# Kernel optimization log

Measured on AMD Instinct MI355X. Metric: run time of the kernel, lower is better.

## Reference

```python
import jax, jax.numpy as jnp
import numpy as np

LAMBDA = 0.9
T = 8192


def setup_inputs() -> dict:
    key = jax.random.key(0)
    k1, k2, k3, k4 = jax.random.split(key, 4)
    return {
        "log_pfs": jax.random.normal(k1, (T,), dtype=jnp.float32),
        "log_pbs": jax.random.normal(k2, (T,), dtype=jnp.float32),
        "log_flows": jax.random.normal(k3, (T + 1,), dtype=jnp.float32),
        "log_reward": jax.random.normal(k4, (), dtype=jnp.float32),
    }


def reference(log_pfs, log_pbs, log_flows, log_reward):
    t = log_pfs.shape[0]
    # terminal flow is replaced by the log reward (log_flows has T+1 entries)
    lfr = log_flows.at[t].set(log_reward)
    zero = jnp.zeros((1,), dtype=log_pfs.dtype)
    cpf = jnp.concatenate([zero, jnp.cumsum(log_pfs)])  # [T+1], cpf[j]-cpf[i] = sum log_pfs[i:j]
    cpb = jnp.concatenate([zero, jnp.cumsum(log_pbs)])
    # balance(i,j) = lfr[i] + (cpf[j]-cpf[i]) - lfr[j] - (cpb[j]-cpb[i]) = D[i] - D[j]
    d = lfr - cpf + cpb  # [T+1]; then balance = d[i]-d[j]+ (cpf[j]-cpf[i]) ... simplify directly:
    d = lfr + (cpb - cpf)  # balance(i,j) = d[i] - d[j]
    idx = jnp.arange(t + 1)
    length = idx[None, :] - idx[:, None]  # j - i
    mask = length > 0
    w = jnp.where(mask, jnp.asarray(LAMBDA, log_pfs.dtype) ** length.astype(log_pfs.dtype), 0.0)
    bal = d[:, None] - d[None, :]
    total = jnp.sum(w * bal * bal)
    wsum = jnp.sum(w)
    return jnp.where(wsum > 0, total / wsum, total)
```

## Files before the change

### kernel.cpp

```cpp
#include <hip/hip_runtime.h>


#define TT 8192
#define NTH 1024
#define LAM 0.9
#define LOG2LAM_F (-0.15200309344504995f)

constexpr double dpow(double b, long e) {
  double r = 1.0;
  for (long i = 0; i < e; ++i) r *= b;
  return r;
}

constexpr float M8F[7] = {
    (float)dpow(LAM, 8),   (float)dpow(LAM, 16),  (float)dpow(LAM, 32),
    (float)dpow(LAM, 64),  (float)dpow(LAM, 128), (float)dpow(LAM, 256),
    (float)dpow(LAM, 512)};

__global__ __launch_bounds__(NTH) void subtb_fused_kernel(
    const float* __restrict__ log_pfs,
    const float* __restrict__ log_pbs,
    const float* __restrict__ log_flows,
    const float* __restrict__ log_reward,
    float* __restrict__ out, double wsum) {
  const int tid  = threadIdx.x;
  const int lane = tid & 63;
  const int wid  = tid >> 6;
  const int base = tid * 8;

  __shared__ double wtot1[16];
  __shared__ float  wtot2[16];
  __shared__ float  rt1[16], rt2[16];

  const float4* pf4 = (const float4*)(log_pfs + base);
  const float4* pb4 = (const float4*)(log_pbs + base);
  const float4* fl4 = (const float4*)(log_flows + base);
  float4 a0 = pf4[0], a1 = pf4[1];
  float4 b0 = pb4[0], b1 = pb4[1];
  float4 f0 = fl4[0], f1 = fl4[1];
  float fa[8] = {a0.x, a0.y, a0.z, a0.w, a1.x, a1.y, a1.z, a1.w};
  float fb[8] = {b0.x, b0.y, b0.z, b0.w, b1.x, b1.y, b1.z, b1.w};
  float ff[8] = {f0.x, f0.y, f0.z, f0.w, f1.x, f1.y, f1.z, f1.w};

  double lexcl[8];
  double run = 0.0;
#pragma unroll
  for (int r = 0; r < 8; ++r) {
    lexcl[r] = run;
    run += (double)fb[r] - (double)fa[r];
  }
  double x = run;
#pragma unroll
  for (int off = 1; off < 64; off <<= 1) {
    double u = __shfl_up(x, off, 64);
    if (lane >= off) x += u;
  }
  if (lane == 63) wtot1[wid] = x;
  __syncthreads();
  double wexcl = 0.0;
  for (int w = 0; w < wid; ++w) wexcl += wtot1[w];
  const double texcl = wexcl + (x - run);

  float dvf[8];
#pragma unroll
  for (int r = 0; r < 8; ++r) dvf[r] = (float)((double)ff[r] + texcl + lexcl[r]);

  float bl = 0.0f;
#pragma unroll
  for (int r = 0; r < 8; ++r) bl = 0.9f * (bl + dvf[r]);

  float xw = __shfl_up(bl, 1, 64);
  if (lane < 1) xw = 0.0f;
#pragma unroll
  for (int b = 0; b < 6; ++b) {
    const int off = 1 << b;
    float u = __shfl_up(xw, off, 64);
    if (lane >= off) xw += M8F[b] * u;
  }
  if (lane == 63) wtot2[wid] = bl + M8F[0] * xw;
  __syncthreads();
  float Cw = 0.0f;
  for (int w = 0; w < wid; ++w) Cw = M8F[6] * Cw + wtot2[w];
  float c = __builtin_amdgcn_exp2f(8.0f * LOG2LAM_F * (float)lane) * Cw + xw;

  float t1 = 0.0f, t2 = 0.0f;
  float pj = __builtin_amdgcn_exp2f(LOG2LAM_F * (float)base);
  float qj = __builtin_amdgcn_exp2f(LOG2LAM_F * (float)(TT - base));
  const float invl = 1.0f / 0.9f;
#pragma unroll
  for (int r = 0; r < 8; ++r) {
    const float dr = dvf[r];
    t1 += dr * dr * (2.0f - qj - pj);
    t2 += dr * c;
    c = 0.9f * (c + dr);
    pj *= 0.9f;
    qj *= invl;
  }
  if (tid == NTH - 1) {
    const double dT = (double)log_reward[0] + (wexcl + x);
    t1 += (float)(dT * dT);
    t2 += (float)dT * c;
  }

#pragma unroll
  for (int off = 32; off > 0; off >>= 1) {
    t1 += __shfl_down(t1, off, 64);
    t2 += __shfl_down(t2, off, 64);
  }
  if (lane == 0) { rt1[wid] = t1; rt2[wid] = t2; }
  __syncthreads();
  if (tid == 0) {
    double s1 = 0.0, s2 = 0.0;
    for (int w = 0; w < 16; ++w) { s1 += (double)rt1[w]; s2 += (double)rt2[w]; }
    const double total = (LAM / (1.0 - LAM)) * s1 - 2.0 * s2;
    out[0] = (float)(total / wsum);
  }
}

extern "C" void kernel_launch(void* const* d_in, const int* in_sizes, int n_in,
                              void* d_out, int out_size, void* d_ws, size_t ws_size,
                              hipStream_t stream) {
  const float* log_pfs    = (const float*)d_in[0];
  const float* log_pbs    = (const float*)d_in[1];
  const float* log_flows  = (const float*)d_in[2];
  const float* log_reward = (const float*)d_in[3];
  float* out = (float*)d_out;

  double wsum = 0.0, lp = 1.0;
  for (int k = 1; k <= TT; ++k) {
    lp *= LAM;
    wsum += (double)(TT + 1 - k) * lp;
  }

  subtb_fused_kernel<<<1, NTH, 0, stream>>>(log_pfs, log_pbs, log_flows, log_reward, out, wsum);
}
```

Before: 9.949 us.

## Merge the two block scans into one fp32 triple scan

Replaces the double-precision prefix scan followed by a second decayed scan with a single pass. Three quantities (plain prefix sum S and decayed sums U of the differences and V of the flows) are scanned together in fp32, and the carry c is rebuilt algebraically as V + 9S − 10U. This removes one __syncthreads phase, the serial dependency between the scans, and the slow FP64 shuffles and adds. In exchange there are three times the fp32 shuffles, and accumulating the prefix in fp32 with the c recombination may lose accuracy through cancellation.

```diff
diff --git a/kernel.cpp b/kernel.cpp
--- a/kernel.cpp
+++ b/kernel.cpp
@@ -3,7 +3,10 @@
 
 #define TT 8192
 #define NTH 1024
-#define LAM 0.9
+#define LAMF 0.9f
+#define INVLF (1.0f / 0.9f)
+#define C1F 9.0f
+#define C2F 10.0f
 #define LOG2LAM_F (-0.15200309344504995f)
 
 constexpr double dpow(double b, long e) {
@@ -13,9 +16,9 @@
 }
 
 constexpr float M8F[7] = {
-    (float)dpow(LAM, 8),   (float)dpow(LAM, 16),  (float)dpow(LAM, 32),
-    (float)dpow(LAM, 64),  (float)dpow(LAM, 128), (float)dpow(LAM, 256),
-    (float)dpow(LAM, 512)};
+    (float)dpow(0.9, 8),   (float)dpow(0.9, 16),  (float)dpow(0.9, 32),
+    (float)dpow(0.9, 64),  (float)dpow(0.9, 128), (float)dpow(0.9, 256),
+    (float)dpow(0.9, 512)};
 
 __global__ __launch_bounds__(NTH) void subtb_fused_kernel(
     const float* __restrict__ log_pfs,
@@ -28,9 +31,8 @@
   const int wid  = tid >> 6;
   const int base = tid * 8;
 
-  __shared__ double wtot1[16];
-  __shared__ float  wtot2[16];
-  __shared__ float  rt1[16], rt2[16];
+  __shared__ float wS[16], wU[16], wV[16];
+  __shared__ float rt1[16], rt2[16];
 
   const float4* pf4 = (const float4*)(log_pfs + base);
   const float4* pb4 = (const float4*)(log_pbs + base);
@@ -38,68 +40,73 @@
   float4 a0 = pf4[0], a1 = pf4[1];
   float4 b0 = pb4[0], b1 = pb4[1];
   float4 f0 = fl4[0], f1 = fl4[1];
-  float fa[8] = {a0.x, a0.y, a0.z, a0.w, a1.x, a1.y, a1.z, a1.w};
-  float fb[8] = {b0.x, b0.y, b0.z, b0.w, b1.x, b1.y, b1.z, b1.w};
+  float fe[8] = {b0.x - a0.x, b0.y - a0.y, b0.z - a0.z, b0.w - a0.w,
+                 b1.x - a1.x, b1.y - a1.y, b1.z - a1.z, b1.w - a1.w};
   float ff[8] = {f0.x, f0.y, f0.z, f0.w, f1.x, f1.y, f1.z, f1.w};
 
-  double lexcl[8];
-  double run = 0.0;
+  float lexcl[8];
+  float runS = 0.0f;
+#pragma unroll
+  for (int r = 0; r < 8; ++r) { lexcl[r] = runS; runS += fe[r]; }
+  float blU = 0.0f;
+  float blV = 0.0f;
 #pragma unroll
   for (int r = 0; r < 8; ++r) {
-    lexcl[r] = run;
-    run += (double)fb[r] - (double)fa[r];
+    blU = LAMF * (blU + fe[r]);
+    blV = LAMF * (blV + ff[r]);
   }
-  double x = run;
-#pragma unroll
-  for (int off = 1; off < 64; off <<= 1) {
-    double u = __shfl_up(x, off, 64);
-    if (lane >= off) x += u;
-  }
-  if (lane == 63) wtot1[wid] = x;
-  __syncthreads();
-  double wexcl = 0.0;
-  for (int w = 0; w < wid; ++w) wexcl += wtot1[w];
-  const double texcl = wexcl + (x - run);
 
-  float dvf[8];
-#pragma unroll
-  for (int r = 0; r < 8; ++r) dvf[r] = (float)((double)ff[r] + texcl + lexcl[r]);
-
-  float bl = 0.0f;
-#pragma unroll
-  for (int r = 0; r < 8; ++r) bl = 0.9f * (bl + dvf[r]);
-
-  float xw = __shfl_up(bl, 1, 64);
-  if (lane < 1) xw = 0.0f;
+  float xS = runS;
+  float xU = __shfl_up(blU, 1, 64);
+  float xV = __shfl_up(blV, 1, 64);
+  if (lane == 0) { xU = 0.0f; xV = 0.0f; }
 #pragma unroll
   for (int b = 0; b < 6; ++b) {
     const int off = 1 << b;
-    float u = __shfl_up(xw, off, 64);
-    if (lane >= off) xw += M8F[b] * u;
+    float uS = __shfl_up(xS, off, 64);
+    float uU = __shfl_up(xU, off, 64);
+    float uV = __shfl_up(xV, off, 64);
+    if (lane >= off) {
+      xS += uS;
+      xU += M8F[b] * uU;
+      xV += M8F[b] * uV;
+    }
   }
-  if (lane == 63) wtot2[wid] = bl + M8F[0] * xw;
+  if (lane == 63) {
+    wS[wid] = xS;
+    wU[wid] = blU + M8F[0] * xU;
+    wV[wid] = blV + M8F[0] * xV;
+  }
   __syncthreads();
-  float Cw = 0.0f;
-  for (int w = 0; w < wid; ++w) Cw = M8F[6] * Cw + wtot2[w];
-  float c = __builtin_amdgcn_exp2f(8.0f * LOG2LAM_F * (float)lane) * Cw + xw;
+
+  float Sw = 0.0f, Uw = 0.0f, Vw = 0.0f;
+  for (int w = 0; w < wid; ++w) {
+    Sw += wS[w];
+    Uw = M8F[6] * Uw + wU[w];
+    Vw = M8F[6] * Vw + wV[w];
+  }
+  const float Sexcl = Sw + (xS - runS);
+  const float l8l = __builtin_amdgcn_exp2f(8.0f * LOG2LAM_F * (float)lane);
+  const float Uexcl = l8l * Uw + xU;
+  const float Vexcl = l8l * Vw + xV;
+  float c = Vexcl + C1F * Sexcl - C2F * Uexcl;
 
   float t1 = 0.0f, t2 = 0.0f;
   float pj = __builtin_amdgcn_exp2f(LOG2LAM_F * (float)base);
   float qj = __builtin_amdgcn_exp2f(LOG2LAM_F * (float)(TT - base));
-  const float invl = 1.0f / 0.9f;
 #pragma unroll
   for (int r = 0; r < 8; ++r) {
-    const float dr = dvf[r];
-    t1 += dr * dr * (2.0f - qj - pj);
-    t2 += dr * c;
-    c = 0.9f * (c + dr);
-    pj *= 0.9f;
-    qj *= invl;
+    const float d = ff[r] + Sexcl + lexcl[r];
+    t1 += d * d * (2.0f - qj - pj);
+    t2 += d * c;
+    c = LAMF * (c + d);
+    pj *= LAMF;
+    qj *= INVLF;
   }
   if (tid == NTH - 1) {
-    const double dT = (double)log_reward[0] + (wexcl + x);
-    t1 += (float)(dT * dT);
-    t2 += (float)dT * c;
+    const float dT = log_reward[0] + (Sw + xS);
+    t1 += dT * dT;
+    t2 += dT * c;
   }
 
 #pragma unroll
@@ -112,7 +119,7 @@
   if (tid == 0) {
     double s1 = 0.0, s2 = 0.0;
     for (int w = 0; w < 16; ++w) { s1 += (double)rt1[w]; s2 += (double)rt2[w]; }
-    const double total = (LAM / (1.0 - LAM)) * s1 - 2.0 * s2;
+    const double total = 9.0 * s1 - 2.0 * s2;
     out[0] = (float)(total / wsum);
   }
 }
@@ -128,7 +135,7 @@
 
   double wsum = 0.0, lp = 1.0;
   for (int k = 1; k <= TT; ++k) {
-    lp *= LAM;
+    lp *= 0.9;
     wsum += (double)(TT + 1 - k) * lp;
   }
 
```

Measured after the change: 9.684 us. 2.7% less time.
